# Optimization experiments

Measured on AMD Instinct MI355X. Metric: run time of the kernel, lower is better.

The kernel has to match this reference:

```python
import jax, jax.numpy as jnp
import numpy as np
from jax import lax

INPUT_SIZE, HIDDEN, LAYERS, OUT = 49, 32, 2, 10
B, T = 512, 1024


def _param(key, shape, fan):
    bound = 1.0 / np.sqrt(fan)
    return jax.random.uniform(key, shape, jnp.float32, -bound, bound)


def setup_inputs() -> dict:
    key = jax.random.key(0)
    ks = jax.random.split(key, 12)
    return {
        "x": jax.random.normal(ks[0], (B, T, INPUT_SIZE), jnp.float32),
        "W_ih0": _param(ks[1], (4 * HIDDEN, INPUT_SIZE), HIDDEN),
        "W_hh0": _param(ks[2], (4 * HIDDEN, HIDDEN), HIDDEN),
        "b_ih0": _param(ks[3], (4 * HIDDEN,), HIDDEN),
        "b_hh0": _param(ks[4], (4 * HIDDEN,), HIDDEN),
        "W_ih1": _param(ks[5], (4 * HIDDEN, HIDDEN), HIDDEN),
        "W_hh1": _param(ks[6], (4 * HIDDEN, HIDDEN), HIDDEN),
        "b_ih1": _param(ks[7], (4 * HIDDEN,), HIDDEN),
        "b_hh1": _param(ks[8], (4 * HIDDEN,), HIDDEN),
        "W_out": _param(ks[9], (OUT, HIDDEN), HIDDEN),
        "b_out": _param(ks[10], (OUT,), HIDDEN),
    }


def _lstm_layer(x_tbd, W_ih, W_hh, b_ih, b_hh):
    # x_tbd: [T, B, D]; PyTorch gate order i, f, g, o stacked along 4H.
    H = W_hh.shape[1]
    # Precompute input contribution for all timesteps in one GEMM.
    xg = jnp.einsum('tbd,gd->tbg', x_tbd, W_ih) + b_ih + b_hh  # [T, B, 4H]

    def step(carry, xg_t):
        h, c = carry
        gates = xg_t + h @ W_hh.T  # [B, 4H]
        i, f, g, o = jnp.split(gates, 4, axis=-1)
        i = jax.nn.sigmoid(i)
        f = jax.nn.sigmoid(f)
        g = jnp.tanh(g)
        o = jax.nn.sigmoid(o)
        c = f * c + i * g
        h = o * jnp.tanh(c)
        return (h, c), h

    Bsz = x_tbd.shape[1]
    init = (jnp.zeros((Bsz, H), x_tbd.dtype), jnp.zeros((Bsz, H), x_tbd.dtype))
    _, hs = lax.scan(step, init, xg)
    return hs  # [T, B, H]


def reference(x, W_ih0, W_hh0, b_ih0, b_hh0, W_ih1, W_hh1, b_ih1, b_hh1, W_out, b_out):
    # Eval-mode forward (inter-layer dropout disabled).
    xt = jnp.transpose(x, (1, 0, 2))  # [T, B, 49]
    h0 = _lstm_layer(xt, W_ih0, W_hh0, b_ih0, b_hh0)  # [T, B, 32]
    h1 = _lstm_layer(h0, W_ih1, W_hh1, b_ih1, b_hh1)  # [T, B, 32]
    r_out = jnp.transpose(h1, (1, 0, 2))  # [B, T, 32]
    return r_out @ W_out.T + b_out  # [B, T, 10]
```

## Files before the change

kernel.cpp:

```cpp
#include <hip/hip_runtime.h>
#include <cstddef>

#define TSTEPS 1024
#define NIN    49
#define HID    32
#define OUTD   10
#define XSTR   52
#define NGRP   256
#define RMASK  15
#define NB     2

typedef float v2f __attribute__((ext_vector_type(2)));

template<int CTRL>
__device__ __forceinline__ float quad(float v) {
    return __int_as_float(__builtin_amdgcn_mov_dpp(__float_as_int(v), CTRL, 0xF, 0xF, true));
}
__device__ __forceinline__ float sigm(float x) {
    return __builtin_amdgcn_rcpf(1.f + __expf(-x));
}
__device__ __forceinline__ void pkfma(v2f& acc, v2f a, v2f b) {
    asm("v_pk_fma_f32 %0, %1, %2, %0" : "+v"(acc) : "v"(a), "v"(b));
}

__device__ __forceinline__ int ldacq(const int* p) {
    return __hip_atomic_load(p, __ATOMIC_ACQUIRE, __HIP_MEMORY_SCOPE_WORKGROUP);
}
__device__ __forceinline__ void pub(int* p, int v, int lane) {
    if (lane == 0)
        __hip_atomic_store(p, v, __ATOMIC_RELEASE, __HIP_MEMORY_SCOPE_WORKGROUP);
}
__device__ __forceinline__ void waitge(const int* p, int need, int& cache) {
    if (cache >= need) return;
    int c = ldacq(p);
    while (c < need) { __builtin_amdgcn_s_sleep(1); c = ldacq(p); }
    cache = c;
}

#define LOADH2(BASE, H2)                                                     \
    v2f H2[8];                                                               \
    {                                                                        \
        const float4* hp_ = (const float4*)(BASE);                           \
        const float4 a_ = hp_[0], b_ = hp_[1], c_ = hp_[2], d_ = hp_[3];     \
        H2[0] = (v2f){a_.x, a_.y}; H2[1] = (v2f){a_.z, a_.w};                \
        H2[2] = (v2f){b_.x, b_.y}; H2[3] = (v2f){b_.z, b_.w};                \
        H2[4] = (v2f){c_.x, c_.y}; H2[5] = (v2f){c_.z, c_.w};                \
        H2[6] = (v2f){d_.x, d_.y}; H2[7] = (v2f){d_.z, d_.w};                \
    }

#define DOTPK(W2, H2, S0, S1, S2, S3)                                        \
    float S0, S1, S2, S3;                                                    \
    {                                                                        \
        v2f p0 = {0.f,0.f}, p1 = {0.f,0.f}, p2 = {0.f,0.f}, p3 = {0.f,0.f}; \
        _Pragma("unroll")                                                    \
        for (int m_ = 0; m_ < 8; ++m_) {                                     \
            pkfma(p0, W2[0][m_], H2[m_]);                                    \
            pkfma(p1, W2[1][m_], H2[m_]);                                    \
            pkfma(p2, W2[2][m_], H2[m_]);                                    \
            pkfma(p3, W2[3][m_], H2[m_]);                                    \
        }                                                                    \
        S0 = p0.x + p0.y; S1 = p1.x + p1.y;                                  \
        S2 = p2.x + p2.y; S3 = p3.x + p3.y;                                  \
        S0 += quad<0xB1>(S0); S1 += quad<0xB1>(S1);                          \
        S2 += quad<0xB1>(S2); S3 += quad<0xB1>(S3);                          \
    }

__device__ __forceinline__ float gate_act(float s0, float s1, float s2, float s3,
                                          int gp, float& c) {
    const float inA = gp ? s2 + s2 : s0;
    const float inB = gp ? s3 : s1;
    const float sA = sigm(inA);
    const float sB = sigm(inB);
    const float vA = gp ? fmaf(2.f, sA, -1.f) : sA;
    const float xA = quad<0xB1>(vA);
    const float xB = quad<0xB1>(sB);
    const float fg = gp ? xB : sB;
    const float og = gp ? sB : xB;
    c = fmaf(fg, c, vA * xA);
    return og * fmaf(2.f, sigm(c + c), -1.f);
}

extern "C" __global__ void __launch_bounds__(512, 1)
lstm_pair8(const float* __restrict__ x,
           const float* __restrict__ Wih0, const float* __restrict__ Whh0,
           const float* __restrict__ bih0, const float* __restrict__ bhh0,
           const float* __restrict__ Wih1, const float* __restrict__ Whh1,
           const float* __restrict__ bih1, const float* __restrict__ bhh1,
           const float* __restrict__ Wout, const float* __restrict__ bout,
           float* __restrict__ y)
{
    const int tid  = threadIdx.x;
    const int lane = tid & 63;
    const int w    = tid >> 6;
    const int bi   = w >> 2;
    const int role = (w & 3) ^ bi;

    __shared__ __align__(16) float xs[NB][2 * 16 * XSTR];
    __shared__ __align__(16) float xg0[NB][16][HID][4];
    __shared__ __align__(16) float xg1[NB][16][HID][4];
    __shared__ __align__(16) float h0r[NB][16][HID];
    __shared__ __align__(16) float h1r[NB][16][HID];
    __shared__ int ctr[NB][5];

    {
        float* z0 = &h0r[0][0][0];
        float* z1 = &h1r[0][0][0];
        for (int i = tid; i < NB * 16 * HID; i += 512) { z0[i] = 0.f; z1[i] = 0.f; }
        if (tid < NB * 5) ctr[tid / 5][tid % 5] = -1;
    }
    __syncthreads();

    const float* __restrict__ xb = x + ((size_t)blockIdx.x * NB + bi) * TSTEPS * NIN;
    float* __restrict__ yb       = y + ((size_t)blockIdx.x * NB + bi) * TSTEPS * OUTD;
    int* cr = &ctr[bi][0];

    if (role == 0) {
        const int j = lane >> 1, gp = lane & 1;
        v2f wh0[4][8];
#pragma unroll
        for (int g = 0; g < 4; ++g) {
            const float* wr = Whh0 + (g * HID + j) * HID + 16 * gp;
#pragma unroll
            for (int m = 0; m < 8; ++m) wh0[g][m] = (v2f){wr[2*m], wr[2*m + 1]};
        }
        float c0 = 0.f;
        int cProd = -1, cQd = -1;
        __builtin_amdgcn_s_setprio(1);
        for (int g = 0; g < NGRP; ++g) {
            if ((g & 1) == 0) {
                waitge(&cr[0], 4 * g + 7, cProd);
                if (g >= 4) waitge(&cr[2], 4 * g - 9, cQd);
            }
#pragma unroll
            for (int u = 0; u < 4; ++u) {
                const int t = 4 * g + u;
                LOADH2(&h0r[bi][(t + RMASK) & RMASK][16 * gp], hv)
                DOTPK(wh0, hv, s0, s1, s2, s3)
                const float4 xg = *(const float4*)&xg0[bi][t & RMASK][j][0];
                const float hval = gate_act(s0 + xg.x, s1 + xg.y,
                                            s2 + xg.z, s3 + xg.w, gp, c0);
                if (gp == 0) h0r[bi][t & RMASK][j] = hval;
            }
            pub(&cr[1], 4 * g + 3, lane);
        }
    } else if (role == 1) {
        const int j = lane >> 1, gp = lane & 1;
        v2f wi1[4][8];
        float b1v[4];
#pragma unroll
        for (int g = 0; g < 4; ++g) {
            const float* wr = Wih1 + (g * HID + j) * HID + 16 * gp;
#pragma unroll
            for (int m = 0; m < 8; ++m) wi1[g][m] = (v2f){wr[2*m], wr[2*m + 1]};
            b1v[g] = bih1[g * HID + j] + bhh1[g * HID + j];
        }
        float wo[8], bo = 0.f;
        const int po = lane >> 2, kq = lane & 3;
        if (lane < 40) {
#pragma unroll
            for (int m = 0; m < 8; ++m) wo[m] = Wout[po * HID + kq * 8 + m];
            bo = bout[po];
        } else {
#pragma unroll
            for (int m = 0; m < 8; ++m) wo[m] = 0.f;
        }
        int cL0 = -1, cL1 = -1;
        for (int g = 0; g < NGRP; ++g) {
            if ((g & 1) == 0) {
                waitge(&cr[1], 4 * g + 7, cL0);
                if (g >= 4) waitge(&cr[3], 4 * g - 9, cL1);
            }
#pragma unroll
            for (int u = 0; u < 4; ++u) {
                const int t = 4 * g + u;
                LOADH2(&h0r[bi][t & RMASK][16 * gp], hq)
                DOTPK(wi1, hq, q0, q1, q2, q3)
                if (gp == 0) {
                    float4 o;
                    o.x = q0 + b1v[0]; o.y = q1 + b1v[1];
                    o.z = q2 + b1v[2]; o.w = q3 + b1v[3];
                    *(float4*)&xg1[bi][t & RMASK][j][0] = o;
                }
            }
            pub(&cr[2], 4 * g + 3, lane);
            if (g >= 4) {
                const int gy = g - 4;
#pragma unroll
                for (int u = 0; u < 4; ++u) {
                    const int ty = 4 * gy + u;
                    const float* hb = &h1r[bi][ty & RMASK][kq * 8];
                    const float4 va = *(const float4*)hb;
                    const float4 vb = *(const float4*)(hb + 4);
                    float acc = wo[0]*va.x + wo[1]*va.y + wo[2]*va.z + wo[3]*va.w
                              + wo[4]*vb.x + wo[5]*vb.y + wo[6]*vb.z + wo[7]*vb.w;
                    acc += quad<0xB1>(acc);
                    acc += quad<0x4E>(acc);
                    if (lane < 40 && kq == 0) yb[(size_t)ty * OUTD + po] = acc + bo;
                }
                pub(&cr[4], 4 * gy + 3, lane);
            }
        }
        for (int gy = NGRP - 4; gy < NGRP; ++gy) {
            waitge(&cr[3], 4 * gy + 3, cL1);
#pragma unroll
            for (int u = 0; u < 4; ++u) {
                const int ty = 4 * gy + u;
                const float* hb = &h1r[bi][ty & RMASK][kq * 8];
                const float4 va = *(const float4*)hb;
                const float4 vb = *(const float4*)(hb + 4);
                float acc = wo[0]*va.x + wo[1]*va.y + wo[2]*va.z + wo[3]*va.w
                          + wo[4]*vb.x + wo[5]*vb.y + wo[6]*vb.z + wo[7]*vb.w;
                acc += quad<0xB1>(acc);
                acc += quad<0x4E>(acc);
                if (lane < 40 && kq == 0) yb[(size_t)ty * OUTD + po] = acc + bo;
            }
            pub(&cr[4], 4 * gy + 3, lane);
        }
    } else if (role == 2) {
        const int j = lane >> 1, gp = lane & 1;
        v2f wh1[4][8];
#pragma unroll
        for (int g = 0; g < 4; ++g) {
            const float* wr = Whh1 + (g * HID + j) * HID + 16 * gp;
#pragma unroll
            for (int m = 0; m < 8; ++m) wh1[g][m] = (v2f){wr[2*m], wr[2*m + 1]};
        }
        float c1 = 0.f;
        int cQd = -1, cPrj = -1;
        __builtin_amdgcn_s_setprio(1);
        for (int g = 0; g < NGRP; ++g) {
            if ((g & 1) == 0) {
                waitge(&cr[2], 4 * g + 7, cQd);
                if (g >= 4) waitge(&cr[4], 4 * g - 9, cPrj);
            }
#pragma unroll
            for (int u = 0; u < 4; ++u) {
                const int t = 4 * g + u;
                LOADH2(&h1r[bi][(t + RMASK) & RMASK][16 * gp], hv)
                DOTPK(wh1, hv, s0, s1, s2, s3)
                const float4 xg = *(const float4*)&xg1[bi][t & RMASK][j][0];
                const float hval = gate_act(s0 + xg.x, s1 + xg.y,
                                            s2 + xg.z, s3 + xg.w, gp, c1);
                if (gp == 0) h1r[bi][t & RMASK][j] = hval;
            }
            pub(&cr[3], 4 * g + 3, lane);
        }
    } else {
        const int jj = lane & 31;
        const int gA = lane >> 5;
        const int gB = 2 + (lane >> 5);

        v2f wa2[24], wb2[24];
        float wa48, wb48, b0a, b0b;
        {
            const float* wra = Wih0 + (gA * HID + jj) * NIN;
            const float* wrb = Wih0 + (gB * HID + jj) * NIN;
#pragma unroll
            for (int m = 0; m < 24; ++m) {
                wa2[m] = (v2f){wra[2*m], wra[2*m + 1]};
                wb2[m] = (v2f){wrb[2*m], wrb[2*m + 1]};
            }
            wa48 = wra[48]; wb48 = wrb[48];
            b0a = bih0[gA * HID + jj] + bhh0[gA * HID + jj];
            b0b = bih0[gB * HID + jj] + bhh0[gB * HID + jj];
        }

        int laddr[13];
#pragma unroll
        for (int r = 0; r < 13; ++r) {
            const int idx = lane + r * 64;
            const int s_  = idx / NIN;
            laddr[r] = s_ * XSTR + (idx - s_ * NIN);
        }
        float xr[13];

        auto issue = [&](int cn) {
            const float* src = xb + (size_t)cn * 16 * NIN;
#pragma unroll
            for (int r = 0; r < 12; ++r) xr[r] = src[lane + r * 64];
            if (lane < 16) xr[12] = src[lane + 768];
        };
        auto drain = [&](int cn) {
            float* dst = &xs[bi][(cn & 1) * (16 * XSTR)];
#pragma unroll
            for (int r = 0; r < 12; ++r) dst[laddr[r]] = xr[r];
            if (lane < 16) dst[laddr[12]] = xr[12];
        };
        auto pdot = [&](int t) {
            const float* xp = &xs[bi][((t >> 4) & 1) * (16 * XSTR) + (t & 15) * XSTR];
            const float4* x4 = (const float4*)xp;
            v2f aA0 = (v2f){b0a, 0.f}, aA1 = (v2f){0.f, 0.f};
            v2f aB0 = (v2f){b0b, 0.f}, aB1 = (v2f){0.f, 0.f};
#pragma unroll
            for (int u = 0; u < 12; ++u) {
                const float4 xv = x4[u];
                const v2f xlo = (v2f){xv.x, xv.y};
                const v2f xhi = (v2f){xv.z, xv.w};
                pkfma(aA0, wa2[2*u],     xlo);
                pkfma(aA1, wa2[2*u + 1], xhi);
                pkfma(aB0, wb2[2*u],     xlo);
                pkfma(aB1, wb2[2*u + 1], xhi);
            }
            const float x48 = xp[48];
            const float a0 = fmaf(wa48, x48, (aA0.x + aA0.y) + (aA1.x + aA1.y));
            const float a2 = fmaf(wb48, x48, (aB0.x + aB0.y) + (aB1.x + aB1.y));
            xg0[bi][t & RMASK][jj][gA] = a0;
            xg0[bi][t & RMASK][jj][gB] = a2;
        };

        issue(0);
        drain(0);

        int cL0 = -1;
        for (int g = 0; g < NGRP; ++g) {
            if ((g & 1) == 0 && g >= 4)
                waitge(&cr[1], 4 * g - 9, cL0);
            const int cn = (g >> 2) + 1;
            if ((g & 3) == 0 && cn < 64) issue(cn);
            pdot(4 * g); pdot(4 * g + 1); pdot(4 * g + 2); pdot(4 * g + 3);
            if ((g & 3) == 2 && cn < 64) drain(cn);
            pub(&cr[0], 4 * g + 3, lane);
        }
    }
}

extern "C" void kernel_launch(void* const* d_in, const int* in_sizes, int n_in,
                              void* d_out, int out_size, void* d_ws, size_t ws_size,
                              hipStream_t stream) {
    (void)in_sizes; (void)n_in; (void)d_ws; (void)ws_size; (void)out_size;
    const float* x    = (const float*)d_in[0];
    const float* Wih0 = (const float*)d_in[1];
    const float* Whh0 = (const float*)d_in[2];
    const float* bih0 = (const float*)d_in[3];
    const float* bhh0 = (const float*)d_in[4];
    const float* Wih1 = (const float*)d_in[5];
    const float* Whh1 = (const float*)d_in[6];
    const float* bih1 = (const float*)d_in[7];
    const float* bhh1 = (const float*)d_in[8];
    const float* Wout = (const float*)d_in[9];
    const float* bout = (const float*)d_in[10];
    float* y = (float*)d_out;

    lstm_pair8<<<dim3(512 / NB), dim3(512), 0, stream>>>(
        x, Wih0, Whh0, bih0, bhh0, Wih1, Whh1, bih1, bhh1, Wout, bout, y);
}
```

Before: 400.6 us.

## Merge input-projection, layer-1 input, and output roles into one wavefront per batch

Reduces each block from 8 to 6 wavefronts by folding the layer-0 input GEMM, the layer-1 input projection, and the output projection into a single software-pipelined wave per sequence. Stages are skewed by 3 and 6 groups, and wait targets are clamped so the final waits cannot deadlock. The goal is fewer wavefronts competing with the two recurrent critical-path waves for SIMD issue slots. The cost is that one wave now does roughly three times the non-recurrent work and may fall behind the recurrence.

Result: slower. 576.4 us (+43.9%).

```diff
diff --git a/kernel.cpp b/kernel.cpp
--- a/kernel.cpp
+++ b/kernel.cpp
@@ -9,6 +9,7 @@
 #define NGRP   256
 #define RMASK  15
 #define NB     2
+#define CMAX   1023
 
 typedef float v2f __attribute__((ext_vector_type(2)));
 
@@ -22,6 +23,7 @@
 __device__ __forceinline__ void pkfma(v2f& acc, v2f a, v2f b) {
     asm("v_pk_fma_f32 %0, %1, %2, %0" : "+v"(acc) : "v"(a), "v"(b));
 }
+__device__ __forceinline__ int imin(int a, int b) { return a < b ? a : b; }
 
 __device__ __forceinline__ int ldacq(const int* p) {
     return __hip_atomic_load(p, __ATOMIC_ACQUIRE, __HIP_MEMORY_SCOPE_WORKGROUP);
@@ -80,20 +82,21 @@
     return og * fmaf(2.f, sigm(c + c), -1.f);
 }
 
-extern "C" __global__ void __launch_bounds__(512, 1)
-lstm_pair8(const float* __restrict__ x,
-           const float* __restrict__ Wih0, const float* __restrict__ Whh0,
-           const float* __restrict__ bih0, const float* __restrict__ bhh0,
-           const float* __restrict__ Wih1, const float* __restrict__ Whh1,
-           const float* __restrict__ bih1, const float* __restrict__ bhh1,
-           const float* __restrict__ Wout, const float* __restrict__ bout,
-           float* __restrict__ y)
+extern "C" __global__ void __launch_bounds__(384, 1)
+lstm_w6(const float* __restrict__ x,
+        const float* __restrict__ Wih0, const float* __restrict__ Whh0,
+        const float* __restrict__ bih0, const float* __restrict__ bhh0,
+        const float* __restrict__ Wih1, const float* __restrict__ Whh1,
+        const float* __restrict__ bih1, const float* __restrict__ bhh1,
+        const float* __restrict__ Wout, const float* __restrict__ bout,
+        float* __restrict__ y)
 {
     const int tid  = threadIdx.x;
     const int lane = tid & 63;
     const int w    = tid >> 6;
-    const int bi   = w >> 2;
-    const int role = (w & 3) ^ bi;
+    const int bi   = (w >= 3);
+    const int wi   = bi ? (w - 3) : w;
+    const int role = bi ? (wi == 0 ? 2 : wi - 1) : wi;
 
     __shared__ __align__(16) float xs[NB][2 * 16 * XSTR];
     __shared__ __align__(16) float xg0[NB][16][HID][4];
@@ -105,7 +108,7 @@
     {
         float* z0 = &h0r[0][0][0];
         float* z1 = &h1r[0][0][0];
-        for (int i = tid; i < NB * 16 * HID; i += 512) { z0[i] = 0.f; z1[i] = 0.f; }
+        for (int i = tid; i < NB * 16 * HID; i += 384) { z0[i] = 0.f; z1[i] = 0.f; }
         if (tid < NB * 5) ctr[tid / 5][tid % 5] = -1;
     }
     __syncthreads();
@@ -128,7 +131,7 @@
         __builtin_amdgcn_s_setprio(1);
         for (int g = 0; g < NGRP; ++g) {
             if ((g & 1) == 0) {
-                waitge(&cr[0], 4 * g + 7, cProd);
+                waitge(&cr[0], imin(4 * g + 7, CMAX), cProd);
                 if (g >= 4) waitge(&cr[2], 4 * g - 9, cQd);
             }
 #pragma unroll
@@ -145,6 +148,36 @@
         }
     } else if (role == 1) {
         const int j = lane >> 1, gp = lane & 1;
+        v2f wh1[4][8];
+#pragma unroll
+        for (int g = 0; g < 4; ++g) {
+            const float* wr = Whh1 + (g * HID + j) * HID + 16 * gp;
+#pragma unroll
+            for (int m = 0; m < 8; ++m) wh1[g][m] = (v2f){wr[2*m], wr[2*m + 1]};
+        }
+        float c1 = 0.f;
+        int cQd = -1, cPrj = -1;
+        __builtin_amdgcn_s_setprio(1);
+        for (int g = 0; g < NGRP; ++g) {
+            if ((g & 1) == 0) {
+                waitge(&cr[2], imin(4 * g + 7, CMAX), cQd);
+                if (g >= 4) waitge(&cr[4], 4 * g - 9, cPrj);
+            }
+#pragma unroll
+            for (int u = 0; u < 4; ++u) {
+                const int t = 4 * g + u;
+                LOADH2(&h1r[bi][(t + RMASK) & RMASK][16 * gp], hv)
+                DOTPK(wh1, hv, s0, s1, s2, s3)
+                const float4 xg = *(const float4*)&xg1[bi][t & RMASK][j][0];
+                const float hval = gate_act(s0 + xg.x, s1 + xg.y,
+                                            s2 + xg.z, s3 + xg.w, gp, c1);
+                if (gp == 0) h1r[bi][t & RMASK][j] = hval;
+            }
+            pub(&cr[3], 4 * g + 3, lane);
+        }
+    } else {
+        const int j = lane >> 1, gp = lane & 1;
+
         v2f wi1[4][8];
         float b1v[4];
 #pragma unroll
@@ -164,27 +197,101 @@
 #pragma unroll
             for (int m = 0; m < 8; ++m) wo[m] = 0.f;
         }
+        const int jj = lane & 31;
+        const int gA = lane >> 5;
+        const int gB = 2 + (lane >> 5);
+        v2f wa2[24], wb2[24];
+        float wa48, wb48, b0a, b0b;
+        {
+            const float* wra = Wih0 + (gA * HID + jj) * NIN;
+            const float* wrb = Wih0 + (gB * HID + jj) * NIN;
+#pragma unroll
+            for (int m = 0; m < 24; ++m) {
+                wa2[m] = (v2f){wra[2*m], wra[2*m + 1]};
+                wb2[m] = (v2f){wrb[2*m], wrb[2*m + 1]};
+            }
+            wa48 = wra[48]; wb48 = wrb[48];
+            b0a = bih0[gA * HID + jj] + bhh0[gA * HID + jj];
+            b0b = bih0[gB * HID + jj] + bhh0[gB * HID + jj];
+        }
+
+        int laddr[13];
+#pragma unroll
+        for (int r = 0; r < 13; ++r) {
+            const int idx = lane + r * 64;
+            const int s_  = idx / NIN;
+            laddr[r] = s_ * XSTR + (idx - s_ * NIN);
+        }
+        float xr[13];
+
+        auto issue = [&](int cn) {
+            const float* src = xb + (size_t)cn * 16 * NIN;
+#pragma unroll
+            for (int r = 0; r < 12; ++r) xr[r] = src[lane + r * 64];
+            if (lane < 16) xr[12] = src[lane + 768];
+        };
+        auto drain = [&](int cn) {
+            float* dst = &xs[bi][(cn & 1) * (16 * XSTR)];
+#pragma unroll
+            for (int r = 0; r < 12; ++r) dst[laddr[r]] = xr[r];
+            if (lane < 16) dst[laddr[12]] = xr[12];
+        };
+        auto pdot = [&](int t) {
+            const float* xp = &xs[bi][((t >> 4) & 1) * (16 * XSTR) + (t & 15) * XSTR];
+            const float4* x4 = (const float4*)xp;
+            v2f aA0 = (v2f){b0a, 0.f}, aA1 = (v2f){0.f, 0.f};
+            v2f aB0 = (v2f){b0b, 0.f}, aB1 = (v2f){0.f, 0.f};
+#pragma unroll
+            for (int u = 0; u < 12; ++u) {
+                const float4 xv = x4[u];
+                const v2f xlo = (v2f){xv.x, xv.y};
+                const v2f xhi = (v2f){xv.z, xv.w};
+                pkfma(aA0, wa2[2*u],     xlo);
+                pkfma(aA1, wa2[2*u + 1], xhi);
+                pkfma(aB0, wb2[2*u],     xlo);
+                pkfma(aB1, wb2[2*u + 1], xhi);
+            }
+            const float x48 = xp[48];
+            const float a0 = fmaf(wa48, x48, (aA0.x + aA0.y) + (aA1.x + aA1.y));
+            const float a2 = fmaf(wb48, x48, (aB0.x + aB0.y) + (aB1.x + aB1.y));
+            xg0[bi][t & RMASK][jj][gA] = a0;
+            xg0[bi][t & RMASK][jj][gB] = a2;
+        };
+
+        issue(0);
+        drain(0);
+
         int cL0 = -1, cL1 = -1;
-        for (int g = 0; g < NGRP; ++g) {
+        for (int g = 0; g < NGRP + 6; ++g) {
             if ((g & 1) == 0) {
-                waitge(&cr[1], 4 * g + 7, cL0);
-                if (g >= 4) waitge(&cr[3], 4 * g - 9, cL1);
-            }
-#pragma unroll
-            for (int u = 0; u < 4; ++u) {
-                const int t = 4 * g + u;
-                LOADH2(&h0r[bi][t & RMASK][16 * gp], hq)
-                DOTPK(wi1, hq, q0, q1, q2, q3)
-                if (gp == 0) {
-                    float4 o;
-                    o.x = q0 + b1v[0]; o.y = q1 + b1v[1];
-                    o.z = q2 + b1v[2]; o.w = q3 + b1v[3];
-                    *(float4*)&xg1[bi][t & RMASK][j][0] = o;
+                if (g >= 2) waitge(&cr[1], imin(4 * g - 5, CMAX), cL0);
+                if (g >= 6) waitge(&cr[3], imin(4 * g - 17, CMAX), cL1);
+            }
+            if (g < NGRP) {
+                const int cn = (g >> 2) + 1;
+                if ((g & 3) == 0 && cn < 64) issue(cn);
+                pdot(4 * g); pdot(4 * g + 1); pdot(4 * g + 2); pdot(4 * g + 3);
+                if ((g & 3) == 2 && cn < 64) drain(cn);
+                pub(&cr[0], 4 * g + 3, lane);
+            }
+            const int gq = g - 3;
+            if (gq >= 0 && gq < NGRP) {
+#pragma unroll
+                for (int u = 0; u < 4; ++u) {
+                    const int t = 4 * gq + u;
+                    LOADH2(&h0r[bi][t & RMASK][16 * gp], hq)
+                    DOTPK(wi1, hq, q0, q1, q2, q3)
+                    if (gp == 0) {
+                        float4 o;
+                        o.x = q0 + b1v[0]; o.y = q1 + b1v[1];
+                        o.z = q2 + b1v[2]; o.w = q3 + b1v[3];
+                        *(float4*)&xg1[bi][t & RMASK][j][0] = o;
+                    }
                 }
-            }
-            pub(&cr[2], 4 * g + 3, lane);
-            if (g >= 4) {
-                const int gy = g - 4;
+                pub(&cr[2], 4 * gq + 3, lane);
+            }
+            const int gy = g - 6;
+            if (gy >= 0 && gy < NGRP) {
 #pragma unroll
                 for (int u = 0; u < 4; ++u) {
                     const int ty = 4 * gy + u;
@@ -199,127 +306,6 @@
                 }
                 pub(&cr[4], 4 * gy + 3, lane);
             }
-        }
-        for (int gy = NGRP - 4; gy < NGRP; ++gy) {
-            waitge(&cr[3], 4 * gy + 3, cL1);
-#pragma unroll
-            for (int u = 0; u < 4; ++u) {
-                const int ty = 4 * gy + u;
-                const float* hb = &h1r[bi][ty & RMASK][kq * 8];
-                const float4 va = *(const float4*)hb;
-                const float4 vb = *(const float4*)(hb + 4);
-                float acc = wo[0]*va.x + wo[1]*va.y + wo[2]*va.z + wo[3]*va.w
-                          + wo[4]*vb.x + wo[5]*vb.y + wo[6]*vb.z + wo[7]*vb.w;
-                acc += quad<0xB1>(acc);
-                acc += quad<0x4E>(acc);
-                if (lane < 40 && kq == 0) yb[(size_t)ty * OUTD + po] = acc + bo;
-            }
-            pub(&cr[4], 4 * gy + 3, lane);
-        }
-    } else if (role == 2) {
-        const int j = lane >> 1, gp = lane & 1;
-        v2f wh1[4][8];
-#pragma unroll
-        for (int g = 0; g < 4; ++g) {
-            const float* wr = Whh1 + (g * HID + j) * HID + 16 * gp;
-#pragma unroll
-            for (int m = 0; m < 8; ++m) wh1[g][m] = (v2f){wr[2*m], wr[2*m + 1]};
-        }
-        float c1 = 0.f;
-        int cQd = -1, cPrj = -1;
-        __builtin_amdgcn_s_setprio(1);
-        for (int g = 0; g < NGRP; ++g) {
-            if ((g & 1) == 0) {
-                waitge(&cr[2], 4 * g + 7, cQd);
-                if (g >= 4) waitge(&cr[4], 4 * g - 9, cPrj);
-            }
-#pragma unroll
-            for (int u = 0; u < 4; ++u) {
-                const int t = 4 * g + u;
-                LOADH2(&h1r[bi][(t + RMASK) & RMASK][16 * gp], hv)
-                DOTPK(wh1, hv, s0, s1, s2, s3)
-                const float4 xg = *(const float4*)&xg1[bi][t & RMASK][j][0];
-                const float hval = gate_act(s0 + xg.x, s1 + xg.y,
-                                            s2 + xg.z, s3 + xg.w, gp, c1);
-                if (gp == 0) h1r[bi][t & RMASK][j] = hval;
-            }
-            pub(&cr[3], 4 * g + 3, lane);
-        }
-    } else {
-        const int jj = lane & 31;
-        const int gA = lane >> 5;
-        const int gB = 2 + (lane >> 5);
-
-        v2f wa2[24], wb2[24];
-        float wa48, wb48, b0a, b0b;
-        {
-            const float* wra = Wih0 + (gA * HID + jj) * NIN;
-            const float* wrb = Wih0 + (gB * HID + jj) * NIN;
-#pragma unroll
-            for (int m = 0; m < 24; ++m) {
-                wa2[m] = (v2f){wra[2*m], wra[2*m + 1]};
-                wb2[m] = (v2f){wrb[2*m], wrb[2*m + 1]};
-            }
-            wa48 = wra[48]; wb48 = wrb[48];
-            b0a = bih0[gA * HID + jj] + bhh0[gA * HID + jj];
-            b0b = bih0[gB * HID + jj] + bhh0[gB * HID + jj];
-        }
-
-        int laddr[13];
-#pragma unroll
-        for (int r = 0; r < 13; ++r) {
-            const int idx = lane + r * 64;
-            const int s_  = idx / NIN;
-            laddr[r] = s_ * XSTR + (idx - s_ * NIN);
-        }
-        float xr[13];
-
-        auto issue = [&](int cn) {
-            const float* src = xb + (size_t)cn * 16 * NIN;
-#pragma unroll
-            for (int r = 0; r < 12; ++r) xr[r] = src[lane + r * 64];
-            if (lane < 16) xr[12] = src[lane + 768];
-        };
-        auto drain = [&](int cn) {
-            float* dst = &xs[bi][(cn & 1) * (16 * XSTR)];
-#pragma unroll
-            for (int r = 0; r < 12; ++r) dst[laddr[r]] = xr[r];
-            if (lane < 16) dst[laddr[12]] = xr[12];
-        };
-        auto pdot = [&](int t) {
-            const float* xp = &xs[bi][((t >> 4) & 1) * (16 * XSTR) + (t & 15) * XSTR];
-            const float4* x4 = (const float4*)xp;
-            v2f aA0 = (v2f){b0a, 0.f}, aA1 = (v2f){0.f, 0.f};
-            v2f aB0 = (v2f){b0b, 0.f}, aB1 = (v2f){0.f, 0.f};
-#pragma unroll
-            for (int u = 0; u < 12; ++u) {
-                const float4 xv = x4[u];
-                const v2f xlo = (v2f){xv.x, xv.y};
-                const v2f xhi = (v2f){xv.z, xv.w};
-                pkfma(aA0, wa2[2*u],     xlo);
-                pkfma(aA1, wa2[2*u + 1], xhi);
-                pkfma(aB0, wb2[2*u],     xlo);
-                pkfma(aB1, wb2[2*u + 1], xhi);
-            }
-            const float x48 = xp[48];
-            const float a0 = fmaf(wa48, x48, (aA0.x + aA0.y) + (aA1.x + aA1.y));
-            const float a2 = fmaf(wb48, x48, (aB0.x + aB0.y) + (aB1.x + aB1.y));
-            xg0[bi][t & RMASK][jj][gA] = a0;
-            xg0[bi][t & RMASK][jj][gB] = a2;
-        };
-
-        issue(0);
-        drain(0);
-
-        int cL0 = -1;
-        for (int g = 0; g < NGRP; ++g) {
-            if ((g & 1) == 0 && g >= 4)
-                waitge(&cr[1], 4 * g - 9, cL0);
-            const int cn = (g >> 2) + 1;
-            if ((g & 3) == 0 && cn < 64) issue(cn);
-            pdot(4 * g); pdot(4 * g + 1); pdot(4 * g + 2); pdot(4 * g + 3);
-            if ((g & 3) == 2 && cn < 64) drain(cn);
-            pub(&cr[0], 4 * g + 3, lane);
         }
     }
 }
@@ -341,6 +327,6 @@
     const float* bout = (const float*)d_in[10];
     float* y = (float*)d_out;
 
-    lstm_pair8<<<dim3(512 / NB), dim3(512), 0, stream>>>(
+    lstm_w6<<<dim3(512 / NB), dim3(384), 0, stream>>>(
         x, Wih0, Whh0, bih0, bhh0, Wih1, Whh1, bih1, bhh1, Wout, bout, y);
 }
```
